# Kernel optimization log

Measured on AMD Instinct MI355X. Metric: run time of the kernel, lower is better.

The kernel has to match this reference:

```python
import jax, jax.numpy as jnp
import numpy as np

BS, ZDIM, HID, TLEN = 1024, 256, 256, 128


def setup_inputs() -> dict:
    key = jax.random.key(0)
    k1, k2, k3 = jax.random.split(key, 3)
    z0 = jax.random.normal(k1, (BS, ZDIM), dtype=jnp.float32)
    # strictly increasing time grid on [0, 1]
    t = jnp.linspace(0.0, 1.0, TLEN).astype(jnp.float32)
    # small init keeps the 127-step RK4 trajectory numerically stable
    W1 = jax.random.normal(k2, (ZDIM, HID), dtype=jnp.float32) * (0.5 / np.sqrt(ZDIM))
    b1 = jnp.zeros((HID,), dtype=jnp.float32)
    W2 = jax.random.normal(k3, (HID, ZDIM), dtype=jnp.float32) * (0.5 / np.sqrt(HID))
    b2 = jnp.zeros((ZDIM,), dtype=jnp.float32)
    return {"z0": z0, "t": t, "W1": W1, "b1": b1, "W2": W2, "b2": b2}


def reference(z0, t, W1, b1, W2, b2):
    # ODEF: f(z, t) = tanh(z @ W1 + b1) @ W2 + b2  (autonomous MLP dynamics)
    def f(z, ti):
        return jnp.tanh(z @ W1 + b1) @ W2 + b2

    def rk4_step(z, ts):
        t0, t1 = ts
        h = t1 - t0
        k1 = f(z, t0)
        k2 = f(z + k1 * (h * 0.5), t0 + h * 0.5)
        k3 = f(z + k2 * (h * 0.5), t0 + h * 0.5)
        k4 = f(z + k3 * h, t0 + h)
        zn = z + (h / 6.0) * (k1 + 2.0 * k2 + 2.0 * k3 + k4)
        return zn, None
    # sequential integration over time_len-1 intervals (matches the python loop)
    zT, _ = jax.lax.scan(rk4_step, z0, (t[:-1], t[1:]))
    # NeuralODE.forward default: return_whole_sequence=False -> z[-1]
    return zT
```

## Files before the change

### kernel.cpp

```cpp
#include <hip/hip_runtime.h>
#include <hip/hip_bf16.h>


#define BS   1024
#define ZDIM 256
#define TLEN 128
#define ROWSTRIDE 264

typedef short v8s __attribute__((ext_vector_type(8)));
typedef float v4f __attribute__((ext_vector_type(4)));

static __device__ __forceinline__ ushort f2bf_rne(float x) {
    union { float f; unsigned u; } v; v.f = x;
    unsigned r = v.u + 0x7FFFu + ((v.u >> 16) & 1u);
    return (ushort)(r >> 16);
}

static __device__ __forceinline__ unsigned pk2(float a, float b) {
    union { __hip_bfloat162 h; unsigned u; } cv;
    cv.h = __float22bfloat162_rn(make_float2(a, b));
    return cv.u;
}

static __device__ __forceinline__ float fast_tanh(float x) {
    float e = __builtin_amdgcn_exp2f(2.88539008177793f * x);
    float r = __builtin_amdgcn_rcpf(e + 1.0f);
    return 1.0f - 2.0f * r;
}

__global__ __launch_bounds__(512, 2)
void ode_mfma_kernel(const float* __restrict__ z0,
                     const float* __restrict__ t,
                     const float* __restrict__ W1,
                     const float* __restrict__ b1,
                     const float* __restrict__ W2,
                     const float* __restrict__ b2,
                     float* __restrict__ out)
{
    __shared__ ushort zbuf[16 * ROWSTRIDE];
    __shared__ ushort hbuf[16 * ROWSTRIDE];
    __shared__ float  hsh[TLEN];

    const int tid  = threadIdx.x;
    const int wv   = tid >> 6;
    const int lane = tid & 63;
    const int q    = lane >> 4;
    const int ln   = lane & 15;
    const int grp  = wv >> 2;
    const int wq   = wv & 3;
    const int rowbase = blockIdx.x * 16;

    if (tid < TLEN - 1) hsh[tid] = t[tid + 1] - t[tid];

    const float* __restrict__ Wsel = grp ? W2 : W1;
    const float* __restrict__ bsel = grp ? b2 : b1;

    v8s wf[4][8];
    #pragma unroll
    for (int ct = 0; ct < 4; ++ct) {
        const int c = wq * 64 + ct * 16 + ln;
        #pragma unroll
        for (int ks = 0; ks < 8; ++ks) {
            v8s a;
            #pragma unroll
            for (int j = 0; j < 8; ++j) {
                const int k = ks * 32 + q * 8 + j;
                a[j] = (short)f2bf_rne(Wsel[k * ZDIM + c]);
            }
            wf[ct][ks] = a;
        }
    }

    v4f bf[4];
    #pragma unroll
    for (int ct = 0; ct < 4; ++ct)
        #pragma unroll
        for (int r = 0; r < 4; ++r)
            bf[ct][r] = bsel[wq * 64 + ct * 16 + q * 4 + r];

    const int rdbase = ln * ROWSTRIDE + q * 8;
    const int wrbase = ln * ROWSTRIDE + wq * 64 + q * 4;

    float zloc[4][4];
    float kacc[4][4];
    if (grp) {
        #pragma unroll
        for (int ct = 0; ct < 4; ++ct) {
            #pragma unroll
            for (int r = 0; r < 4; ++r)
                zloc[ct][r] = z0[(rowbase + ln) * ZDIM + wq * 64 + ct * 16 + q * 4 + r];
            uint2 p; p.x = pk2(zloc[ct][0], zloc[ct][1]); p.y = pk2(zloc[ct][2], zloc[ct][3]);
            *(uint2*)&zbuf[wrbase + ct * 16] = p;
        }
    }
    __syncthreads();

    #pragma unroll 1
    for (int step = 0; step < TLEN - 1; ++step) {
        const float h = hsh[step];

        #pragma unroll
        for (int stage = 0; stage < 4; ++stage) {
            if (!grp) {
                v4f a0 = bf[0], a1 = bf[1], a2 = bf[2], a3 = bf[3];
                #pragma unroll
                for (int ks = 0; ks < 8; ++ks) {
                    const v8s zf = *(const v8s*)&zbuf[rdbase + ks * 32];
                    a0 = __builtin_amdgcn_mfma_f32_16x16x32_bf16(wf[0][ks], zf, a0, 0, 0, 0);
                    a1 = __builtin_amdgcn_mfma_f32_16x16x32_bf16(wf[1][ks], zf, a1, 0, 0, 0);
                    a2 = __builtin_amdgcn_mfma_f32_16x16x32_bf16(wf[2][ks], zf, a2, 0, 0, 0);
                    a3 = __builtin_amdgcn_mfma_f32_16x16x32_bf16(wf[3][ks], zf, a3, 0, 0, 0);
                }
                uint2 p0, p1, p2, p3;
                p0.x = pk2(fast_tanh(a0[0]), fast_tanh(a0[1]));
                p0.y = pk2(fast_tanh(a0[2]), fast_tanh(a0[3]));
                p1.x = pk2(fast_tanh(a1[0]), fast_tanh(a1[1]));
                p1.y = pk2(fast_tanh(a1[2]), fast_tanh(a1[3]));
                p2.x = pk2(fast_tanh(a2[0]), fast_tanh(a2[1]));
                p2.y = pk2(fast_tanh(a2[2]), fast_tanh(a2[3]));
                p3.x = pk2(fast_tanh(a3[0]), fast_tanh(a3[1]));
                p3.y = pk2(fast_tanh(a3[2]), fast_tanh(a3[3]));
                *(uint2*)&hbuf[wrbase]      = p0;
                *(uint2*)&hbuf[wrbase + 16] = p1;
                *(uint2*)&hbuf[wrbase + 32] = p2;
                *(uint2*)&hbuf[wrbase + 48] = p3;
            }
            __syncthreads();

            if (grp) {
                v4f f0 = bf[0], f1 = bf[1], f2 = bf[2], f3 = bf[3];
                #pragma unroll
                for (int ks = 0; ks < 8; ++ks) {
                    const v8s hf = *(const v8s*)&hbuf[rdbase + ks * 32];
                    f0 = __builtin_amdgcn_mfma_f32_16x16x32_bf16(wf[0][ks], hf, f0, 0, 0, 0);
                    f1 = __builtin_amdgcn_mfma_f32_16x16x32_bf16(wf[1][ks], hf, f1, 0, 0, 0);
                    f2 = __builtin_amdgcn_mfma_f32_16x16x32_bf16(wf[2][ks], hf, f2, 0, 0, 0);
                    f3 = __builtin_amdgcn_mfma_f32_16x16x32_bf16(wf[3][ks], hf, f3, 0, 0, 0);
                }
                v4f fa[4] = { f0, f1, f2, f3 };
                #pragma unroll
                for (int ct = 0; ct < 4; ++ct) {
                    float zn[4];
                    #pragma unroll
                    for (int r = 0; r < 4; ++r) {
                        const float f = fa[ct][r];
                        if (stage == 0) {
                            kacc[ct][r] = f;
                            zn[r] = zloc[ct][r] + 0.5f * h * f;
                        } else if (stage == 1) {
                            kacc[ct][r] += 2.0f * f;
                            zn[r] = zloc[ct][r] + 0.5f * h * f;
                        } else if (stage == 2) {
                            kacc[ct][r] += 2.0f * f;
                            zn[r] = zloc[ct][r] + h * f;
                        } else {
                            kacc[ct][r] += f;
                            zloc[ct][r] += (h * (1.0f / 6.0f)) * kacc[ct][r];
                            zn[r] = zloc[ct][r];
                        }
                    }
                    uint2 p; p.x = pk2(zn[0], zn[1]); p.y = pk2(zn[2], zn[3]);
                    *(uint2*)&zbuf[wrbase + ct * 16] = p;
                }
            }
            __syncthreads();
        }
    }

    if (grp) {
        #pragma unroll
        for (int ct = 0; ct < 4; ++ct)
            #pragma unroll
            for (int r = 0; r < 4; ++r)
                out[(rowbase + ln) * ZDIM + wq * 64 + ct * 16 + q * 4 + r] = zloc[ct][r];
    }
}

extern "C" void kernel_launch(void* const* d_in, const int* in_sizes, int n_in,
                              void* d_out, int out_size, void* d_ws, size_t ws_size,
                              hipStream_t stream) {
    const float* z0 = (const float*)d_in[0];
    const float* t  = (const float*)d_in[1];
    const float* W1 = (const float*)d_in[2];
    const float* b1 = (const float*)d_in[3];
    const float* W2 = (const float*)d_in[4];
    const float* b2 = (const float*)d_in[5];
    float* out = (float*)d_out;

    dim3 grid(BS / 16);
    dim3 block(512);
    hipLaunchKernelGGL(ode_mfma_kernel, grid, block, 0, stream,
                       z0, t, W1, b1, W2, b2, out);
}
```

Measured before the change: 642.6 us.

## Split both MLP layers across all eight waves with swizzled LDS addressing

Every one of the eight waves now computes a 32-column slice of both layers, instead of four waves doing layer 1 and four doing layer 2 while the other half idles. This halves the serial MFMA chain per wave in each stage. The K loop is split into two independent accumulator chains to shorten dependency latency. LDS reads and writes use an XOR/rotation-style swizzle to reduce bank conflicts. Each wave now holds both W1 and W2 fragments, so register pressure stays about the same.

```diff
diff --git a/kernel.cpp b/kernel.cpp
--- a/kernel.cpp
+++ b/kernel.cpp
@@ -46,54 +46,66 @@
     const int lane = tid & 63;
     const int q    = lane >> 4;
     const int ln   = lane & 15;
-    const int grp  = wv >> 2;
-    const int wq   = wv & 3;
+    const int l3   = ln & 7;
     const int rowbase = blockIdx.x * 16;
 
     if (tid < TLEN - 1) hsh[tid] = t[tid + 1] - t[tid];
 
-    const float* __restrict__ Wsel = grp ? W2 : W1;
-    const float* __restrict__ bsel = grp ? b2 : b1;
-
-    v8s wf[4][8];
-    #pragma unroll
-    for (int ct = 0; ct < 4; ++ct) {
-        const int c = wq * 64 + ct * 16 + ln;
+    v8s w1f[2][8], w2f[2][8];
+    #pragma unroll
+    for (int ct = 0; ct < 2; ++ct) {
+        const int c = wv * 32 + ct * 16 + ln;
         #pragma unroll
         for (int ks = 0; ks < 8; ++ks) {
-            v8s a;
+            v8s a, b;
             #pragma unroll
             for (int j = 0; j < 8; ++j) {
                 const int k = ks * 32 + q * 8 + j;
-                a[j] = (short)f2bf_rne(Wsel[k * ZDIM + c]);
-            }
-            wf[ct][ks] = a;
+                a[j] = (short)f2bf_rne(W1[k * ZDIM + c]);
+                b[j] = (short)f2bf_rne(W2[k * ZDIM + c]);
+            }
+            w1f[ct][ks] = a;
+            w2f[ct][ks] = b;
         }
     }
 
-    v4f bf[4];
-    #pragma unroll
-    for (int ct = 0; ct < 4; ++ct)
+    v4f b1f[2], b2f[2];
+    #pragma unroll
+    for (int ct = 0; ct < 2; ++ct)
+        #pragma unroll
+        for (int r = 0; r < 4; ++r) {
+            b1f[ct][r] = b1[wv * 32 + ct * 16 + q * 4 + r];
+            b2f[ct][r] = b2[wv * 32 + ct * 16 + q * 4 + r];
+        }
+
+    int rdaddr[8];
+    #pragma unroll
+    for (int ks = 0; ks < 8; ++ks) {
+        const int u  = q + 4 * ks;
+        const int up = (u & 24) | ((u - 2 * l3) & 7);
+        rdaddr[ks] = ln * ROWSTRIDE + up * 8;
+    }
+    int wraddr[2];
+    #pragma unroll
+    for (int ct = 0; ct < 2; ++ct) {
+        const int u  = 4 * wv + 2 * ct + (q >> 1);
+        const int up = (u & 24) | ((u - 2 * l3) & 7);
+        wraddr[ct] = ln * ROWSTRIDE + up * 8 + (q & 1) * 4;
+    }
+
+    float zloc[2][4];
+    #pragma unroll
+    for (int ct = 0; ct < 2; ++ct) {
         #pragma unroll
         for (int r = 0; r < 4; ++r)
-            bf[ct][r] = bsel[wq * 64 + ct * 16 + q * 4 + r];
-
-    const int rdbase = ln * ROWSTRIDE + q * 8;
-    const int wrbase = ln * ROWSTRIDE + wq * 64 + q * 4;
-
-    float zloc[4][4];
-    float kacc[4][4];
-    if (grp) {
-        #pragma unroll
-        for (int ct = 0; ct < 4; ++ct) {
-            #pragma unroll
-            for (int r = 0; r < 4; ++r)
-                zloc[ct][r] = z0[(rowbase + ln) * ZDIM + wq * 64 + ct * 16 + q * 4 + r];
-            uint2 p; p.x = pk2(zloc[ct][0], zloc[ct][1]); p.y = pk2(zloc[ct][2], zloc[ct][3]);
-            *(uint2*)&zbuf[wrbase + ct * 16] = p;
-        }
+            zloc[ct][r] = z0[(rowbase + ln) * ZDIM + wv * 32 + ct * 16 + q * 4 + r];
+        uint2 p; p.x = pk2(zloc[ct][0], zloc[ct][1]); p.y = pk2(zloc[ct][2], zloc[ct][3]);
+        *(uint2*)&zbuf[wraddr[ct]] = p;
     }
     __syncthreads();
+
+    float kacc[2][4];
+    const v4f vz = { 0.f, 0.f, 0.f, 0.f };
 
     #pragma unroll 1
     for (int step = 0; step < TLEN - 1; ++step) {
@@ -101,79 +113,82 @@
 
         #pragma unroll
         for (int stage = 0; stage < 4; ++stage) {
-            if (!grp) {
-                v4f a0 = bf[0], a1 = bf[1], a2 = bf[2], a3 = bf[3];
+            v4f a0A = b1f[0], a1A = b1f[1], a0B = vz, a1B = vz;
+            #pragma unroll
+            for (int ks = 0; ks < 4; ++ks) {
+                const v8s zf = *(const v8s*)&zbuf[rdaddr[ks]];
+                a0A = __builtin_amdgcn_mfma_f32_16x16x32_bf16(w1f[0][ks], zf, a0A, 0, 0, 0);
+                a1A = __builtin_amdgcn_mfma_f32_16x16x32_bf16(w1f[1][ks], zf, a1A, 0, 0, 0);
+            }
+            #pragma unroll
+            for (int ks = 4; ks < 8; ++ks) {
+                const v8s zf = *(const v8s*)&zbuf[rdaddr[ks]];
+                a0B = __builtin_amdgcn_mfma_f32_16x16x32_bf16(w1f[0][ks], zf, a0B, 0, 0, 0);
+                a1B = __builtin_amdgcn_mfma_f32_16x16x32_bf16(w1f[1][ks], zf, a1B, 0, 0, 0);
+            }
+            const v4f acc0 = a0A + a0B;
+            const v4f acc1 = a1A + a1B;
+
+            {
+                uint2 p0, p1;
+                p0.x = pk2(fast_tanh(acc0[0]), fast_tanh(acc0[1]));
+                p0.y = pk2(fast_tanh(acc0[2]), fast_tanh(acc0[3]));
+                p1.x = pk2(fast_tanh(acc1[0]), fast_tanh(acc1[1]));
+                p1.y = pk2(fast_tanh(acc1[2]), fast_tanh(acc1[3]));
+                *(uint2*)&hbuf[wraddr[0]] = p0;
+                *(uint2*)&hbuf[wraddr[1]] = p1;
+            }
+            __syncthreads();
+
+            v4f f0A = b2f[0], f1A = b2f[1], f0B = vz, f1B = vz;
+            #pragma unroll
+            for (int ks = 0; ks < 4; ++ks) {
+                const v8s hf = *(const v8s*)&hbuf[rdaddr[ks]];
+                f0A = __builtin_amdgcn_mfma_f32_16x16x32_bf16(w2f[0][ks], hf, f0A, 0, 0, 0);
+                f1A = __builtin_amdgcn_mfma_f32_16x16x32_bf16(w2f[1][ks], hf, f1A, 0, 0, 0);
+            }
+            #pragma unroll
+            for (int ks = 4; ks < 8; ++ks) {
+                const v8s hf = *(const v8s*)&hbuf[rdaddr[ks]];
+                f0B = __builtin_amdgcn_mfma_f32_16x16x32_bf16(w2f[0][ks], hf, f0B, 0, 0, 0);
+                f1B = __builtin_amdgcn_mfma_f32_16x16x32_bf16(w2f[1][ks], hf, f1B, 0, 0, 0);
+            }
+            const v4f fv0 = f0A + f0B;
+            const v4f fv1 = f1A + f1B;
+
+            #pragma unroll
+            for (int ct = 0; ct < 2; ++ct) {
+                float zn[4];
                 #pragma unroll
-                for (int ks = 0; ks < 8; ++ks) {
-                    const v8s zf = *(const v8s*)&zbuf[rdbase + ks * 32];
-                    a0 = __builtin_amdgcn_mfma_f32_16x16x32_bf16(wf[0][ks], zf, a0, 0, 0, 0);
-                    a1 = __builtin_amdgcn_mfma_f32_16x16x32_bf16(wf[1][ks], zf, a1, 0, 0, 0);
-                    a2 = __builtin_amdgcn_mfma_f32_16x16x32_bf16(wf[2][ks], zf, a2, 0, 0, 0);
-                    a3 = __builtin_amdgcn_mfma_f32_16x16x32_bf16(wf[3][ks], zf, a3, 0, 0, 0);
+                for (int r = 0; r < 4; ++r) {
+                    const float f = (ct == 0) ? fv0[r] : fv1[r];
+                    if (stage == 0) {
+                        kacc[ct][r] = f;
+                        zn[r] = zloc[ct][r] + 0.5f * h * f;
+                    } else if (stage == 1) {
+                        kacc[ct][r] += 2.0f * f;
+                        zn[r] = zloc[ct][r] + 0.5f * h * f;
+                    } else if (stage == 2) {
+                        kacc[ct][r] += 2.0f * f;
+                        zn[r] = zloc[ct][r] + h * f;
+                    } else {
+                        kacc[ct][r] += f;
+                        zloc[ct][r] += (h * (1.0f / 6.0f)) * kacc[ct][r];
+                        zn[r] = zloc[ct][r];
+                    }
                 }
-                uint2 p0, p1, p2, p3;
-                p0.x = pk2(fast_tanh(a0[0]), fast_tanh(a0[1]));
-                p0.y = pk2(fast_tanh(a0[2]), fast_tanh(a0[3]));
-                p1.x = pk2(fast_tanh(a1[0]), fast_tanh(a1[1]));
-                p1.y = pk2(fast_tanh(a1[2]), fast_tanh(a1[3]));
-                p2.x = pk2(fast_tanh(a2[0]), fast_tanh(a2[1]));
-                p2.y = pk2(fast_tanh(a2[2]), fast_tanh(a2[3]));
-                p3.x = pk2(fast_tanh(a3[0]), fast_tanh(a3[1]));
-                p3.y = pk2(fast_tanh(a3[2]), fast_tanh(a3[3]));
-                *(uint2*)&hbuf[wrbase]      = p0;
-                *(uint2*)&hbuf[wrbase + 16] = p1;
-                *(uint2*)&hbuf[wrbase + 32] = p2;
-                *(uint2*)&hbuf[wrbase + 48] = p3;
-            }
-            __syncthreads();
-
-            if (grp) {
-                v4f f0 = bf[0], f1 = bf[1], f2 = bf[2], f3 = bf[3];
-                #pragma unroll
-                for (int ks = 0; ks < 8; ++ks) {
-                    const v8s hf = *(const v8s*)&hbuf[rdbase + ks * 32];
-                    f0 = __builtin_amdgcn_mfma_f32_16x16x32_bf16(wf[0][ks], hf, f0, 0, 0, 0);
-                    f1 = __builtin_amdgcn_mfma_f32_16x16x32_bf16(wf[1][ks], hf, f1, 0, 0, 0);
-                    f2 = __builtin_amdgcn_mfma_f32_16x16x32_bf16(wf[2][ks], hf, f2, 0, 0, 0);
-                    f3 = __builtin_amdgcn_mfma_f32_16x16x32_bf16(wf[3][ks], hf, f3, 0, 0, 0);
-                }
-                v4f fa[4] = { f0, f1, f2, f3 };
-                #pragma unroll
-                for (int ct = 0; ct < 4; ++ct) {
-                    float zn[4];
-                    #pragma unroll
-                    for (int r = 0; r < 4; ++r) {
-                        const float f = fa[ct][r];
-                        if (stage == 0) {
-                            kacc[ct][r] = f;
-                            zn[r] = zloc[ct][r] + 0.5f * h * f;
-                        } else if (stage == 1) {
-                            kacc[ct][r] += 2.0f * f;
-                            zn[r] = zloc[ct][r] + 0.5f * h * f;
-                        } else if (stage == 2) {
-                            kacc[ct][r] += 2.0f * f;
-                            zn[r] = zloc[ct][r] + h * f;
-                        } else {
-                            kacc[ct][r] += f;
-                            zloc[ct][r] += (h * (1.0f / 6.0f)) * kacc[ct][r];
-                            zn[r] = zloc[ct][r];
-                        }
-                    }
-                    uint2 p; p.x = pk2(zn[0], zn[1]); p.y = pk2(zn[2], zn[3]);
-                    *(uint2*)&zbuf[wrbase + ct * 16] = p;
-                }
+                uint2 p; p.x = pk2(zn[0], zn[1]); p.y = pk2(zn[2], zn[3]);
+                *(uint2*)&zbuf[wraddr[ct]] = p;
             }
             __syncthreads();
         }
     }
 
-    if (grp) {
-        #pragma unroll
-        for (int ct = 0; ct < 4; ++ct)
-            #pragma unroll
-            for (int r = 0; r < 4; ++r)
-                out[(rowbase + ln) * ZDIM + wq * 64 + ct * 16 + q * 4 + r] = zloc[ct][r];
-    }
+    #pragma unroll
+    for (int ct = 0; ct < 2; ++ct)
+        #pragma unroll
+        for (int r = 0; r < 4; ++r)
+            out[(rowbase + ln) * ZDIM + wv * 32 + ct * 16 + q * 4 + r] = zloc[ct][r];
 }
 
 extern "C" void kernel_launch(void* const* d_in, const int* in_sizes, int n_in,
```

Result: faster. 621.6 us (-3.3%).
